# Kernel tuning notes

Hardware: AMD Instinct MI355X
Metric: run time of the kernel (lower is better)

The kernel has to match this reference:

```python
import jax, jax.numpy as jnp
import numpy as np

N = 50000        # total nodes (2 node types x 25000)
NPER = 25000     # nodes per type
E = 600000       # edges
R = 8            # num relations
NB = 4           # num bases
IND = 256        # raw input dim per node type
HID = 128        # hidden_dim
OUT = 64         # out_dim


def setup_inputs() -> dict:
    key = jax.random.key(0)
    ks = jax.random.split(key, 24)
    s_in = 1.0 / np.sqrt(IND)
    s_h = 1.0 / np.sqrt(HID)
    d = {
        "x_paper": jax.random.normal(ks[0], (NPER, IND), jnp.float32),
        "x_author": jax.random.normal(ks[1], (NPER, IND), jnp.float32),
        "W_paper": jax.random.normal(ks[2], (IND, HID), jnp.float32) * s_in,
        "b_paper": jnp.zeros((HID,), jnp.float32),
        "W_author": jax.random.normal(ks[3], (IND, HID), jnp.float32) * s_in,
        "b_author": jnp.zeros((HID,), jnp.float32),
        "bases0": jax.random.normal(ks[4], (NB, HID, HID), jnp.float32) * s_h,
        "comp0": jax.random.normal(ks[5], (R, NB), jnp.float32) * (1.0 / np.sqrt(NB)),
        "root0": jax.random.normal(ks[6], (HID, HID), jnp.float32) * s_h,
        "bias0": jnp.zeros((HID,), jnp.float32),
        "bases1": jax.random.normal(ks[7], (NB, HID, HID), jnp.float32) * s_h,
        "comp1": jax.random.normal(ks[8], (R, NB), jnp.float32) * (1.0 / np.sqrt(NB)),
        "root1": jax.random.normal(ks[9], (HID, HID), jnp.float32) * s_h,
        "bias1": jnp.zeros((HID,), jnp.float32),
        "bases2": jax.random.normal(ks[10], (NB, HID, OUT), jnp.float32) * s_h,
        "comp2": jax.random.normal(ks[11], (R, NB), jnp.float32) * (1.0 / np.sqrt(NB)),
        "root2": jax.random.normal(ks[12], (HID, OUT), jnp.float32) * s_h,
        "bias2": jnp.zeros((OUT,), jnp.float32),
        "edge_index": jax.random.randint(ks[13], (2, E), 0, N, dtype=jnp.int64),
        "edge_type": jax.random.randint(ks[14], (E,), 0, R, dtype=jnp.int64),
    }
    return d


def rgcn_conv(x, src, dst, etype, bases, comp, root, bias):
    # weight[r] = sum_b comp[r,b] * bases[b]  -> [R, in, out]
    W = jnp.einsum('rb,bio->rio', comp, bases)
    # per-(dst node, relation) mean aggregation (PyG RGCNConv default aggr='mean')
    seg = dst * R + etype                                   # [E]
    cnt = jax.ops.segment_sum(jnp.ones((E,), x.dtype), seg, num_segments=N * R)
    norm = 1.0 / jnp.maximum(cnt, 1.0)                      # [N*R]
    msg = x[src] * norm[seg][:, None]                       # [E, in]
    agg = jax.ops.segment_sum(msg, seg, num_segments=N * R) # [N*R, in]
    agg = agg.reshape(N, R, x.shape[1])                     # [N, R, in]
    return jnp.einsum('nri,rio->no', agg, W) + x @ root + bias


def reference(x_paper, x_author, W_paper, b_paper, W_author, b_author,
              bases0, comp0, root0, bias0,
              bases1, comp1, root1, bias1,
              bases2, comp2, root2, bias2,
              edge_index, edge_type):
    # Lazy linear projections + ReLU (dropout is identity in eval mode)
    hp = jax.nn.relu(x_paper @ W_paper + b_paper)
    ha = jax.nn.relu(x_author @ W_author + b_author)
    x = jnp.concatenate([hp, ha], axis=0)                   # [N, HID]

    src, dst = edge_index[0], edge_index[1]
    x_latents = [x]

    # conv 0 (i == 0: replace)
    h = jax.nn.relu(rgcn_conv(x, src, dst, edge_type, bases0, comp0, root0, bias0))
    x_latents.append(x)
    x = h

    # conv 1 (i > 0: residual add)
    h = jax.nn.relu(rgcn_conv(x, src, dst, edge_type, bases1, comp1, root1, bias1))
    x_latents.append(x)
    x = x + h

    # final conv
    out = rgcn_conv(x, src, dst, edge_type, bases2, comp2, root2, bias2)
    return (out, x_latents)
```

## Files before the change

kernel.cpp:

```cpp
#include <hip/hip_runtime.h>
#include <stdint.h>

#define NPER  25000
#define NNODE 50000
#define NEDGE 600000
#define NREL  8
#define NBASE 4
#define INDIM 256
#define HIDD  128
#define OUTD  64
#define NSEG  (NNODE * NREL)

typedef unsigned short u16;
typedef unsigned int   u32;
typedef __attribute__((ext_vector_type(8))) __bf16          bf16x8;
typedef __attribute__((ext_vector_type(8))) unsigned short  ushort8;
typedef __attribute__((ext_vector_type(4))) float           f32x4;

__device__ __forceinline__ u16 f2b(float f) {
    union { __bf16 h; u16 u; } v; v.h = (__bf16)f; return v.u;
}
__device__ __forceinline__ bf16x8 as_bf(ushort8 u) {
    union { ushort8 a; bf16x8 b; } v; v.a = u; return v.b;
}
__device__ __forceinline__ bf16x8 cvt8(const float* p) {
    f32x4 f0 = *(const f32x4*)p;
    f32x4 f1 = *(const f32x4*)(p + 4);
    ushort8 u;
#pragma unroll
    for (int i = 0; i < 4; i++) { u[i] = f2b(f0[i]); u[i + 4] = f2b(f1[i]); }
    return as_bf(u);
}
__device__ __forceinline__ float blo(u32 v) {
    union { u32 i; float f; } u; u.i = v << 16; return u.f;
}
__device__ __forceinline__ float bhi(u32 v) {
    union { u32 i; float f; } u; u.i = v & 0xffff0000u; return u.f;
}

__global__ void build_bsw_proj(const float* __restrict__ W, int K, u16* __restrict__ Bsw) {
    int idx = blockIdx.x * blockDim.x + threadIdx.x;
    if (idx >= K * 128) return;
    int j    = idx & 7;
    int lane = (idx >> 3) & 63;
    int rest = idx >> 9;
    int nt   = rest & 7;
    int ks   = rest >> 3;
    int col  = nt * 16 + (lane & 15);
    int k    = ks * 32 + ((lane >> 4) << 3) + j;
    Bsw[idx] = f2b(W[(size_t)k * 128 + col]);
}

__global__ void build_bsw_conv(const float* __restrict__ bases, const float* __restrict__ root,
                               int ncol, u16* __restrict__ Bsw) {
    int idx = blockIdx.x * blockDim.x + threadIdx.x;
    if (idx >= 640 * ncol) return;
    int nt_cnt = ncol >> 4;
    int j    = idx & 7;
    int lane = (idx >> 3) & 63;
    int rest = idx >> 9;
    int nt   = rest % nt_cnt;
    int ks   = rest / nt_cnt;
    int col  = nt * 16 + (lane & 15);
    int k    = ks * 32 + ((lane >> 4) << 3) + j;
    float v = (k < 512) ? bases[(size_t)k * ncol + col] : root[(size_t)(k - 512) * ncol + col];
    Bsw[idx] = f2b(v);
}

__global__ void hist_kernel(const int* __restrict__ ei, const int* __restrict__ et,
                            int* __restrict__ cnt) {
    int e = blockIdx.x * blockDim.x + threadIdx.x;
    if (e >= NEDGE) return;
    int dst = ei[NEDGE + e];
    int r   = et[e];
    atomicAdd(&cnt[dst * NREL + r], 1);
}

#define SCAN_CHUNK 1024
__global__ void scan1_kernel(int* __restrict__ data, int n, int* __restrict__ bsum) {
    __shared__ int sh[256];
    int t = threadIdx.x;
    int base = blockIdx.x * SCAN_CHUNK + t * 4;
    int v[4];
#pragma unroll
    for (int i = 0; i < 4; i++) v[i] = (base + i < n) ? data[base + i] : 0;
    int tot = v[0] + v[1] + v[2] + v[3];
    sh[t] = tot; __syncthreads();
    for (int off = 1; off < 256; off <<= 1) {
        int x = (t >= off) ? sh[t - off] : 0;
        __syncthreads();
        sh[t] += x;
        __syncthreads();
    }
    int excl = sh[t] - tot;
    if (t == 255) bsum[blockIdx.x] = sh[255];
    int run = excl;
#pragma unroll
    for (int i = 0; i < 4; i++) {
        if (base + i < n) data[base + i] = run;
        run += v[i];
    }
}

__global__ void scan2_kernel(int* __restrict__ bsum, int nb) {
    __shared__ int sh[512];
    int t = threadIdx.x;
    int v = (t < nb) ? bsum[t] : 0;
    sh[t] = v; __syncthreads();
    for (int off = 1; off < 512; off <<= 1) {
        int x = (t >= off) ? sh[t - off] : 0;
        __syncthreads();
        sh[t] += x;
        __syncthreads();
    }
    if (t < nb) bsum[t] = sh[t] - v;
}

__global__ void scan3_kernel(int* __restrict__ data, int n, const int* __restrict__ bsum) {
    int add = bsum[blockIdx.x];
    int base = blockIdx.x * SCAN_CHUNK + threadIdx.x * 4;
#pragma unroll
    for (int i = 0; i < 4; i++)
        if (base + i < n) data[base + i] += add;
}

__global__ void scatter_kernel(const int* __restrict__ ei, const int* __restrict__ et,
                               int* __restrict__ fill, int* __restrict__ epk) {
    int e = blockIdx.x * blockDim.x + threadIdx.x;
    if (e >= NEDGE) return;
    int src = ei[e];
    int dst = ei[NEDGE + e];
    int r   = et[e];
    int pos = atomicAdd(&fill[dst * NREL + r], 1);
    epk[pos] = src | (r << 16);
}

__global__ __launch_bounds__(256) void agg_kernel(
    const u16* __restrict__ xbf, const float* __restrict__ comp,
    const int* __restrict__ rowptr, const int* __restrict__ epk,
    u16* __restrict__ Abuf) {
    __shared__ float wtab[4][32];
    int tid  = threadIdx.x;
    int wv   = __builtin_amdgcn_readfirstlane(tid >> 6);
    int lane = tid & 63;
    int node = blockIdx.x * 4 + wv;
    int rbase = node * NREL;
    if (lane < 32) {
        int r  = lane >> 2;
        int c0 = rowptr[rbase + r], c1 = rowptr[rbase + r + 1];
        int cnt = c1 - c0;
        float nrm = (cnt > 0) ? 1.f / (float)cnt : 0.f;
        wtab[wv][lane] = comp[lane] * nrm;
    }
    __syncthreads();
    const float* wt = &wtab[wv][0];
    int p = rowptr[rbase];
    int e = rowptr[rbase + 8];
    int co = lane * 2;
    float a0[4] = {0.f, 0.f, 0.f, 0.f};
    float a1[4] = {0.f, 0.f, 0.f, 0.f};
    while (p + 4 <= e) {
        int k0 = epk[p], k1 = epk[p + 1], k2 = epk[p + 2], k3 = epk[p + 3];
        u32 v0 = *(const u32*)(xbf + ((size_t)(k0 & 0xffff) << 7) + co);
        u32 v1 = *(const u32*)(xbf + ((size_t)(k1 & 0xffff) << 7) + co);
        u32 v2 = *(const u32*)(xbf + ((size_t)(k2 & 0xffff) << 7) + co);
        u32 v3 = *(const u32*)(xbf + ((size_t)(k3 & 0xffff) << 7) + co);
        f32x4 w0 = *(const f32x4*)(wt + ((k0 >> 16) << 2));
        f32x4 w1 = *(const f32x4*)(wt + ((k1 >> 16) << 2));
        f32x4 w2 = *(const f32x4*)(wt + ((k2 >> 16) << 2));
        f32x4 w3 = *(const f32x4*)(wt + ((k3 >> 16) << 2));
        float x00 = blo(v0), x01 = bhi(v0);
        float x10 = blo(v1), x11 = bhi(v1);
        float x20 = blo(v2), x21 = bhi(v2);
        float x30 = blo(v3), x31 = bhi(v3);
#pragma unroll
        for (int b = 0; b < 4; b++) {
            a0[b] += w0[b] * x00; a1[b] += w0[b] * x01;
            a0[b] += w1[b] * x10; a1[b] += w1[b] * x11;
            a0[b] += w2[b] * x20; a1[b] += w2[b] * x21;
            a0[b] += w3[b] * x30; a1[b] += w3[b] * x31;
        }
        p += 4;
    }
    while (p < e) {
        int k0 = epk[p];
        u32 v0 = *(const u32*)(xbf + ((size_t)(k0 & 0xffff) << 7) + co);
        f32x4 w0 = *(const f32x4*)(wt + ((k0 >> 16) << 2));
        float x00 = blo(v0), x01 = bhi(v0);
#pragma unroll
        for (int b = 0; b < 4; b++) { a0[b] += w0[b] * x00; a1[b] += w0[b] * x01; }
        p++;
    }
    size_t ob = (size_t)node * 512 + co;
#pragma unroll
    for (int b = 0; b < 4; b++) {
        u32 pk = (u32)f2b(a0[b]) | ((u32)f2b(a1[b]) << 16);
        *(u32*)(Abuf + ob + b * 128) = pk;
    }
}

template<int KMAIN, bool HASX, int NT, bool RELU, bool RES, bool AF32>
__global__ __launch_bounds__(256) void gemm_kernel(
    const void* __restrict__ Av, const u16* __restrict__ xq,
    const u16* __restrict__ Bsw, const float* __restrict__ bias, int M,
    float* __restrict__ out1, float* __restrict__ out2, u16* __restrict__ outb,
    const float* __restrict__ resid, int ldo) {
    constexpr int KSM = KMAIN / 32;
    constexpr int KST = KSM + (HASX ? 4 : 0);
    int tid  = threadIdx.x;
    int wave = tid >> 6, lane = tid & 63;
    int l15  = lane & 15, quad = lane >> 4;
    int rowA = blockIdx.x * 64 + wave * 16 + l15;
    if (rowA > M - 1) rowA = M - 1;
    const u16* bp = Bsw + lane * 8;
    f32x4 acc[NT];
#pragma unroll
    for (int i = 0; i < NT; i++) acc[i] = (f32x4){0.f, 0.f, 0.f, 0.f};
#pragma unroll
    for (int ks = 0; ks < KST; ks++) {
        bf16x8 a;
        if (ks < KSM) {
            if (AF32) a = cvt8((const float*)Av + (size_t)rowA * KMAIN + ks * 32 + quad * 8);
            else      a = as_bf(*(const ushort8*)((const u16*)Av + (size_t)rowA * KMAIN + ks * 32 + quad * 8));
        } else {
            a = as_bf(*(const ushort8*)(xq + (size_t)rowA * 128 + (ks - KSM) * 32 + quad * 8));
        }
#pragma unroll
        for (int nt = 0; nt < NT; nt++) {
            bf16x8 b = as_bf(*(const ushort8*)(bp + ((size_t)(ks * NT + nt) << 9)));
            acc[nt] = __builtin_amdgcn_mfma_f32_16x16x32_bf16(a, b, acc[nt], 0, 0, 0);
        }
    }
    int orow0 = blockIdx.x * 64 + wave * 16 + quad * 4;
#pragma unroll
    for (int r = 0; r < 4; r++) {
        int orow = orow0 + r;
        if (orow < M) {
#pragma unroll
            for (int nt = 0; nt < NT; nt++) {
                int col = nt * 16 + l15;
                float v = acc[nt][r] + bias[col];
                if (RELU) v = v > 0.f ? v : 0.f;
                if (RES)  v += resid[(size_t)orow * ldo + col];
                size_t oi = (size_t)orow * ldo + col;
                if (out1) out1[oi] = v;
                if (out2) out2[oi] = v;
                if (outb) outb[oi] = f2b(v);
            }
        }
    }
}

extern "C" void kernel_launch(void* const* d_in, const int* in_sizes, int n_in,
                              void* d_out, int out_size, void* d_ws, size_t ws_size,
                              hipStream_t stream) {
    const float* x_paper  = (const float*)d_in[0];
    const float* x_author = (const float*)d_in[1];
    const float* W_paper  = (const float*)d_in[2];
    const float* b_paper  = (const float*)d_in[3];
    const float* W_author = (const float*)d_in[4];
    const float* b_author = (const float*)d_in[5];
    const float* bases0   = (const float*)d_in[6];
    const float* comp0    = (const float*)d_in[7];
    const float* root0    = (const float*)d_in[8];
    const float* bias0    = (const float*)d_in[9];
    const float* bases1   = (const float*)d_in[10];
    const float* comp1    = (const float*)d_in[11];
    const float* root1    = (const float*)d_in[12];
    const float* bias1    = (const float*)d_in[13];
    const float* bases2   = (const float*)d_in[14];
    const float* comp2    = (const float*)d_in[15];
    const float* root2    = (const float*)d_in[16];
    const float* bias2    = (const float*)d_in[17];
    const int* ei         = (const int*)d_in[18];
    const int* et         = (const int*)d_in[19];

    float* ob   = (float*)d_out;
    float* outF = ob;
    float* lat0 = ob + 3200000;
    float* lat1 = ob + 9600000;
    float* lat2 = ob + 16000000;

    char* w = (char*)d_ws;
    u16*   Abuf   = (u16*)(w + 0);
    u16*   xbf0   = (u16*)(w + 51200000);
    u16*   xbf1   = (u16*)(w + 64000000);
    u16*   Bswc   = (u16*)(w + 76800000);
    u16*   Bswp   = (u16*)(w + 76963840);
    u16*   Bswa   = (u16*)(w + 77029376);
    int*   rowptr = (int*)(w + 77094912);
    int*   fill   = (int*)(w + 78694976);
    int*   epk    = (int*)(w + 80294976);
    int*   bsum   = (int*)(w + 82694976);

    build_bsw_proj<<<(INDIM * HIDD + 255) / 256, 256, 0, stream>>>(W_paper, INDIM, Bswp);
    build_bsw_proj<<<(INDIM * HIDD + 255) / 256, 256, 0, stream>>>(W_author, INDIM, Bswa);
    gemm_kernel<256, false, 8, true, false, true><<<(NPER + 63) / 64, 256, 0, stream>>>(
        x_paper, nullptr, Bswp, b_paper, NPER, lat0, lat1, xbf0, nullptr, HIDD);
    gemm_kernel<256, false, 8, true, false, true><<<(NPER + 63) / 64, 256, 0, stream>>>(
        x_author, nullptr, Bswa, b_author, NPER,
        lat0 + (size_t)NPER * HIDD, lat1 + (size_t)NPER * HIDD,
        xbf0 + (size_t)NPER * HIDD, nullptr, HIDD);

    hipMemsetAsync(rowptr, 0, (NSEG + 1) * sizeof(int), stream);
    hist_kernel<<<(NEDGE + 255) / 256, 256, 0, stream>>>(ei, et, rowptr);
    int nchunk = (NSEG + 1 + SCAN_CHUNK - 1) / SCAN_CHUNK;
    scan1_kernel<<<nchunk, 256, 0, stream>>>(rowptr, NSEG + 1, bsum);
    scan2_kernel<<<1, 512, 0, stream>>>(bsum, nchunk);
    scan3_kernel<<<nchunk, 256, 0, stream>>>(rowptr, NSEG + 1, bsum);
    hipMemcpyAsync(fill, rowptr, NSEG * sizeof(int), hipMemcpyDeviceToDevice, stream);
    scatter_kernel<<<(NEDGE + 255) / 256, 256, 0, stream>>>(ei, et, fill, epk);

    build_bsw_conv<<<(640 * HIDD + 255) / 256, 256, 0, stream>>>(bases0, root0, HIDD, Bswc);
    agg_kernel<<<NNODE / 4, 256, 0, stream>>>(xbf0, comp0, rowptr, epk, Abuf);
    gemm_kernel<512, true, 8, true, false, false><<<(NNODE + 63) / 64, 256, 0, stream>>>(
        Abuf, xbf0, Bswc, bias0, NNODE, lat2, nullptr, xbf1, nullptr, HIDD);

    build_bsw_conv<<<(640 * HIDD + 255) / 256, 256, 0, stream>>>(bases1, root1, HIDD, Bswc);
    agg_kernel<<<NNODE / 4, 256, 0, stream>>>(xbf1, comp1, rowptr, epk, Abuf);
    gemm_kernel<512, true, 8, true, true, false><<<(NNODE + 63) / 64, 256, 0, stream>>>(
        Abuf, xbf1, Bswc, bias1, NNODE, nullptr, nullptr, xbf0, lat2, HIDD);

    build_bsw_conv<<<(640 * OUTD + 255) / 256, 256, 0, stream>>>(bases2, root2, OUTD, Bswc);
    agg_kernel<<<NNODE / 4, 256, 0, stream>>>(xbf0, comp2, rowptr, epk, Abuf);
    gemm_kernel<512, true, 4, false, false, false><<<(NNODE + 63) / 64, 256, 0, stream>>>(
        Abuf, xbf0, Bswc, bias2, NNODE, outF, nullptr, nullptr, nullptr, OUTD);
}
```

Baseline: 465.8 us.

## Merge weight prep and projections, pipeline aggregation loads, retile conv GEMMs

Puts all five weight-swizzle builds into one launch and both input projections into one 2D-grid launch. The rowptr-to-fill device copy is folded into the last scan pass. The aggregation loop is software-pipelined, prefetching the next four edges' indices and features while the current ones are accumulated, with padded invalid entries in place of a scalar tail loop. The conv GEMMs now run 2 waves per block with each wave computing two 16-row tiles, reusing each B fragment across both tiles at the cost of more registers per wave.

```diff
diff --git a/kernel.cpp b/kernel.cpp
--- a/kernel.cpp
+++ b/kernel.cpp
@@ -38,9 +38,7 @@
     union { u32 i; float f; } u; u.i = v & 0xffff0000u; return u.f;
 }
 
-__global__ void build_bsw_proj(const float* __restrict__ W, int K, u16* __restrict__ Bsw) {
-    int idx = blockIdx.x * blockDim.x + threadIdx.x;
-    if (idx >= K * 128) return;
+__device__ __forceinline__ void bsw_proj_elem(const float* __restrict__ W, u16* __restrict__ out, int idx) {
     int j    = idx & 7;
     int lane = (idx >> 3) & 63;
     int rest = idx >> 9;
@@ -48,13 +46,10 @@
     int ks   = rest >> 3;
     int col  = nt * 16 + (lane & 15);
     int k    = ks * 32 + ((lane >> 4) << 3) + j;
-    Bsw[idx] = f2b(W[(size_t)k * 128 + col]);
-}
-
-__global__ void build_bsw_conv(const float* __restrict__ bases, const float* __restrict__ root,
-                               int ncol, u16* __restrict__ Bsw) {
-    int idx = blockIdx.x * blockDim.x + threadIdx.x;
-    if (idx >= 640 * ncol) return;
+    out[idx] = f2b(W[(size_t)k * 128 + col]);
+}
+__device__ __forceinline__ void bsw_conv_elem(const float* __restrict__ bases, const float* __restrict__ root,
+                                              int ncol, u16* __restrict__ out, int idx) {
     int nt_cnt = ncol >> 4;
     int j    = idx & 7;
     int lane = (idx >> 3) & 63;
@@ -64,7 +59,20 @@
     int col  = nt * 16 + (lane & 15);
     int k    = ks * 32 + ((lane >> 4) << 3) + j;
     float v = (k < 512) ? bases[(size_t)k * ncol + col] : root[(size_t)(k - 512) * ncol + col];
-    Bsw[idx] = f2b(v);
+    out[idx] = f2b(v);
+}
+__global__ void build_bsw_all(const float* __restrict__ Wp, const float* __restrict__ Wa,
+                              const float* __restrict__ bases0, const float* __restrict__ root0,
+                              const float* __restrict__ bases1, const float* __restrict__ root1,
+                              const float* __restrict__ bases2, const float* __restrict__ root2,
+                              u16* __restrict__ Bswp, u16* __restrict__ Bswa,
+                              u16* __restrict__ Bswc0, u16* __restrict__ Bswc1, u16* __restrict__ Bswc2) {
+    int b = blockIdx.x, t = threadIdx.x;
+    if (b < 128)       bsw_proj_elem(Wp, Bswp, b * 256 + t);
+    else if (b < 256)  bsw_proj_elem(Wa, Bswa, (b - 128) * 256 + t);
+    else if (b < 576)  bsw_conv_elem(bases0, root0, HIDD, Bswc0, (b - 256) * 256 + t);
+    else if (b < 896)  bsw_conv_elem(bases1, root1, HIDD, Bswc1, (b - 576) * 256 + t);
+    else               bsw_conv_elem(bases2, root2, OUTD, Bswc2, (b - 896) * 256 + t);
 }
 
 __global__ void hist_kernel(const int* __restrict__ ei, const int* __restrict__ et,
@@ -116,12 +124,19 @@
     if (t < nb) bsum[t] = sh[t] - v;
 }
 
-__global__ void scan3_kernel(int* __restrict__ data, int n, const int* __restrict__ bsum) {
+__global__ void scan3_kernel(int* __restrict__ data, int n, const int* __restrict__ bsum,
+                             int* __restrict__ fill) {
     int add = bsum[blockIdx.x];
     int base = blockIdx.x * SCAN_CHUNK + threadIdx.x * 4;
 #pragma unroll
-    for (int i = 0; i < 4; i++)
-        if (base + i < n) data[base + i] += add;
+    for (int i = 0; i < 4; i++) {
+        int idx = base + i;
+        if (idx < n) {
+            int v = data[idx] + add;
+            data[idx] = v;
+            if (idx < NSEG) fill[idx] = v;
+        }
+    }
 }
 
 __global__ void scatter_kernel(const int* __restrict__ ei, const int* __restrict__ et,
@@ -139,57 +154,52 @@
     const u16* __restrict__ xbf, const float* __restrict__ comp,
     const int* __restrict__ rowptr, const int* __restrict__ epk,
     u16* __restrict__ Abuf) {
-    __shared__ float wtab[4][32];
+    __shared__ float wtab[4][40];
     int tid  = threadIdx.x;
     int wv   = __builtin_amdgcn_readfirstlane(tid >> 6);
     int lane = tid & 63;
     int node = blockIdx.x * 4 + wv;
     int rbase = node * NREL;
-    if (lane < 32) {
-        int r  = lane >> 2;
-        int c0 = rowptr[rbase + r], c1 = rowptr[rbase + r + 1];
-        int cnt = c1 - c0;
-        float nrm = (cnt > 0) ? 1.f / (float)cnt : 0.f;
-        wtab[wv][lane] = comp[lane] * nrm;
+    if (lane < 36) {
+        float wval = 0.f;
+        if (lane < 32) {
+            int r  = lane >> 2;
+            int c0 = rowptr[rbase + r], c1 = rowptr[rbase + r + 1];
+            int cnt = c1 - c0;
+            float nrm = (cnt > 0) ? 1.f / (float)cnt : 0.f;
+            wval = comp[lane] * nrm;
+        }
+        wtab[wv][lane] = wval;
     }
     __syncthreads();
     const float* wt = &wtab[wv][0];
-    int p = rowptr[rbase];
-    int e = rowptr[rbase + 8];
+    int p = __builtin_amdgcn_readfirstlane(rowptr[rbase]);
+    int e = __builtin_amdgcn_readfirstlane(rowptr[rbase + 8]);
     int co = lane * 2;
+    const int INV = 8 << 16;
     float a0[4] = {0.f, 0.f, 0.f, 0.f};
     float a1[4] = {0.f, 0.f, 0.f, 0.f};
-    while (p + 4 <= e) {
-        int k0 = epk[p], k1 = epk[p + 1], k2 = epk[p + 2], k3 = epk[p + 3];
-        u32 v0 = *(const u32*)(xbf + ((size_t)(k0 & 0xffff) << 7) + co);
-        u32 v1 = *(const u32*)(xbf + ((size_t)(k1 & 0xffff) << 7) + co);
-        u32 v2 = *(const u32*)(xbf + ((size_t)(k2 & 0xffff) << 7) + co);
-        u32 v3 = *(const u32*)(xbf + ((size_t)(k3 & 0xffff) << 7) + co);
-        f32x4 w0 = *(const f32x4*)(wt + ((k0 >> 16) << 2));
-        f32x4 w1 = *(const f32x4*)(wt + ((k1 >> 16) << 2));
-        f32x4 w2 = *(const f32x4*)(wt + ((k2 >> 16) << 2));
-        f32x4 w3 = *(const f32x4*)(wt + ((k3 >> 16) << 2));
-        float x00 = blo(v0), x01 = bhi(v0);
-        float x10 = blo(v1), x11 = bhi(v1);
-        float x20 = blo(v2), x21 = bhi(v2);
-        float x30 = blo(v3), x31 = bhi(v3);
-#pragma unroll
-        for (int b = 0; b < 4; b++) {
-            a0[b] += w0[b] * x00; a1[b] += w0[b] * x01;
-            a0[b] += w1[b] * x10; a1[b] += w1[b] * x11;
-            a0[b] += w2[b] * x20; a1[b] += w2[b] * x21;
-            a0[b] += w3[b] * x30; a1[b] += w3[b] * x31;
-        }
-        p += 4;
-    }
-    while (p < e) {
-        int k0 = epk[p];
-        u32 v0 = *(const u32*)(xbf + ((size_t)(k0 & 0xffff) << 7) + co);
-        f32x4 w0 = *(const f32x4*)(wt + ((k0 >> 16) << 2));
-        float x00 = blo(v0), x01 = bhi(v0);
-#pragma unroll
-        for (int b = 0; b < 4; b++) { a0[b] += w0[b] * x00; a1[b] += w0[b] * x01; }
-        p++;
+    int k0[4]; u32 v0[4];
+#pragma unroll
+    for (int i = 0; i < 4; i++) k0[i] = (p + i < e) ? epk[p + i] : INV;
+#pragma unroll
+    for (int i = 0; i < 4; i++) v0[i] = *(const u32*)(xbf + ((size_t)(k0[i] & 0xffff) << 7) + co);
+    for (int pc = p; pc < e; pc += 4) {
+        int pn = pc + 4;
+        int k1[4]; u32 v1[4];
+#pragma unroll
+        for (int i = 0; i < 4; i++) k1[i] = (pn + i < e) ? epk[pn + i] : INV;
+#pragma unroll
+        for (int i = 0; i < 4; i++) v1[i] = *(const u32*)(xbf + ((size_t)(k1[i] & 0xffff) << 7) + co);
+#pragma unroll
+        for (int i = 0; i < 4; i++) {
+            f32x4 w = *(const f32x4*)(wt + ((k0[i] >> 16) << 2));
+            float xl = blo(v0[i]), xh = bhi(v0[i]);
+#pragma unroll
+            for (int b = 0; b < 4; b++) { a0[b] += w[b] * xl; a1[b] += w[b] * xh; }
+        }
+#pragma unroll
+        for (int i = 0; i < 4; i++) { k0[i] = k1[i]; v0[i] = v1[i]; }
     }
     size_t ob = (size_t)node * 512 + co;
 #pragma unroll
@@ -199,9 +209,9 @@
     }
 }
 
-template<int KMAIN, bool HASX, int NT, bool RELU, bool RES, bool AF32>
-__global__ __launch_bounds__(256) void gemm_kernel(
-    const void* __restrict__ Av, const u16* __restrict__ xq,
+template<int KMAIN, bool HASX, int NW, int MW, int NT, bool RELU, bool RES, bool AF32>
+__device__ __forceinline__ void gemm_core(
+    int blk, const void* __restrict__ Av, const u16* __restrict__ xq,
     const u16* __restrict__ Bsw, const float* __restrict__ bias, int M,
     float* __restrict__ out1, float* __restrict__ out2, u16* __restrict__ outb,
     const float* __restrict__ resid, int ldo) {
@@ -210,45 +220,84 @@
     int tid  = threadIdx.x;
     int wave = tid >> 6, lane = tid & 63;
     int l15  = lane & 15, quad = lane >> 4;
-    int rowA = blockIdx.x * 64 + wave * 16 + l15;
-    if (rowA > M - 1) rowA = M - 1;
+    int rowbase = blk * (NW * MW * 16) + wave * (MW * 16);
+    int rA[MW];
+#pragma unroll
+    for (int m = 0; m < MW; m++) {
+        rA[m] = rowbase + m * 16 + l15;
+        if (rA[m] > M - 1) rA[m] = M - 1;
+    }
     const u16* bp = Bsw + lane * 8;
-    f32x4 acc[NT];
-#pragma unroll
-    for (int i = 0; i < NT; i++) acc[i] = (f32x4){0.f, 0.f, 0.f, 0.f};
+    f32x4 acc[MW][NT];
+#pragma unroll
+    for (int m = 0; m < MW; m++)
+#pragma unroll
+        for (int i = 0; i < NT; i++) acc[m][i] = (f32x4){0.f, 0.f, 0.f, 0.f};
 #pragma unroll
     for (int ks = 0; ks < KST; ks++) {
-        bf16x8 a;
-        if (ks < KSM) {
-            if (AF32) a = cvt8((const float*)Av + (size_t)rowA * KMAIN + ks * 32 + quad * 8);
-            else      a = as_bf(*(const ushort8*)((const u16*)Av + (size_t)rowA * KMAIN + ks * 32 + quad * 8));
-        } else {
-            a = as_bf(*(const ushort8*)(xq + (size_t)rowA * 128 + (ks - KSM) * 32 + quad * 8));
+        bf16x8 a[MW];
+#pragma unroll
+        for (int m = 0; m < MW; m++) {
+            if (ks < KSM) {
+                if (AF32) a[m] = cvt8((const float*)Av + (size_t)rA[m] * KMAIN + ks * 32 + quad * 8);
+                else      a[m] = as_bf(*(const ushort8*)((const u16*)Av + (size_t)rA[m] * KMAIN + ks * 32 + quad * 8));
+            } else {
+                a[m] = as_bf(*(const ushort8*)(xq + (size_t)rA[m] * 128 + (ks - KSM) * 32 + quad * 8));
+            }
         }
 #pragma unroll
         for (int nt = 0; nt < NT; nt++) {
             bf16x8 b = as_bf(*(const ushort8*)(bp + ((size_t)(ks * NT + nt) << 9)));
-            acc[nt] = __builtin_amdgcn_mfma_f32_16x16x32_bf16(a, b, acc[nt], 0, 0, 0);
-        }
-    }
-    int orow0 = blockIdx.x * 64 + wave * 16 + quad * 4;
-#pragma unroll
-    for (int r = 0; r < 4; r++) {
-        int orow = orow0 + r;
-        if (orow < M) {
-#pragma unroll
-            for (int nt = 0; nt < NT; nt++) {
-                int col = nt * 16 + l15;
-                float v = acc[nt][r] + bias[col];
-                if (RELU) v = v > 0.f ? v : 0.f;
-                if (RES)  v += resid[(size_t)orow * ldo + col];
-                size_t oi = (size_t)orow * ldo + col;
-                if (out1) out1[oi] = v;
-                if (out2) out2[oi] = v;
-                if (outb) outb[oi] = f2b(v);
+#pragma unroll
+            for (int m = 0; m < MW; m++)
+                acc[m][nt] = __builtin_amdgcn_mfma_f32_16x16x32_bf16(a[m], b, acc[m][nt], 0, 0, 0);
+        }
+    }
+#pragma unroll
+    for (int m = 0; m < MW; m++) {
+        int orow0 = rowbase + m * 16 + quad * 4;
+#pragma unroll
+        for (int r = 0; r < 4; r++) {
+            int orow = orow0 + r;
+            if (orow < M) {
+#pragma unroll
+                for (int nt = 0; nt < NT; nt++) {
+                    int col = nt * 16 + l15;
+                    float v = acc[m][nt][r] + bias[col];
+                    if (RELU) v = v > 0.f ? v : 0.f;
+                    if (RES)  v += resid[(size_t)orow * ldo + col];
+                    size_t oi = (size_t)orow * ldo + col;
+                    if (out1) out1[oi] = v;
+                    if (out2) out2[oi] = v;
+                    if (outb) outb[oi] = f2b(v);
+                }
             }
         }
     }
+}
+
+template<int KMAIN, bool HASX, int NW, int MW, int NT, bool RELU, bool RES, bool AF32>
+__global__ __launch_bounds__(NW * 64, 2) void gemm_kernel(
+    const void* __restrict__ Av, const u16* __restrict__ xq,
+    const u16* __restrict__ Bsw, const float* __restrict__ bias, int M,
+    float* __restrict__ out1, float* __restrict__ out2, u16* __restrict__ outb,
+    const float* __restrict__ resid, int ldo) {
+    gemm_core<KMAIN, HASX, NW, MW, NT, RELU, RES, AF32>(
+        blockIdx.x, Av, xq, Bsw, bias, M, out1, out2, outb, resid, ldo);
+}
+
+__global__ __launch_bounds__(256, 2) void proj2_kernel(
+    const float* __restrict__ xp, const float* __restrict__ xa,
+    const u16* __restrict__ Bswp, const u16* __restrict__ Bswa,
+    const float* __restrict__ bp, const float* __restrict__ ba,
+    float* __restrict__ lat0, float* __restrict__ lat1, u16* __restrict__ xbf0) {
+    int y = blockIdx.y;
+    const float* A    = y ? xa : xp;
+    const u16*   B    = y ? Bswa : Bswp;
+    const float* bias = y ? ba : bp;
+    size_t off = (size_t)y * NPER * HIDD;
+    gemm_core<256, false, 4, 1, 8, true, false, true>(
+        blockIdx.x, A, nullptr, B, bias, NPER, lat0 + off, lat1 + off, xbf0 + off, nullptr, HIDD);
 }
 
 extern "C" void kernel_launch(void* const* d_in, const int* in_sizes, int n_in,
@@ -285,44 +334,40 @@
     u16*   Abuf   = (u16*)(w + 0);
     u16*   xbf0   = (u16*)(w + 51200000);
     u16*   xbf1   = (u16*)(w + 64000000);
-    u16*   Bswc   = (u16*)(w + 76800000);
-    u16*   Bswp   = (u16*)(w + 76963840);
-    u16*   Bswa   = (u16*)(w + 77029376);
-    int*   rowptr = (int*)(w + 77094912);
-    int*   fill   = (int*)(w + 78694976);
-    int*   epk    = (int*)(w + 80294976);
-    int*   bsum   = (int*)(w + 82694976);
-
-    build_bsw_proj<<<(INDIM * HIDD + 255) / 256, 256, 0, stream>>>(W_paper, INDIM, Bswp);
-    build_bsw_proj<<<(INDIM * HIDD + 255) / 256, 256, 0, stream>>>(W_author, INDIM, Bswa);
-    gemm_kernel<256, false, 8, true, false, true><<<(NPER + 63) / 64, 256, 0, stream>>>(
-        x_paper, nullptr, Bswp, b_paper, NPER, lat0, lat1, xbf0, nullptr, HIDD);
-    gemm_kernel<256, false, 8, true, false, true><<<(NPER + 63) / 64, 256, 0, stream>>>(
-        x_author, nullptr, Bswa, b_author, NPER,
-        lat0 + (size_t)NPER * HIDD, lat1 + (size_t)NPER * HIDD,
-        xbf0 + (size_t)NPER * HIDD, nullptr, HIDD);
+    u16*   Bswc0  = (u16*)(w + 76800000);
+    u16*   Bswc1  = (u16*)(w + 76963840);
+    u16*   Bswc2  = (u16*)(w + 77127680);
+    u16*   Bswp   = (u16*)(w + 77209600);
+    u16*   Bswa   = (u16*)(w + 77275136);
+    int*   rowptr = (int*)(w + 77340672);
+    int*   fill   = (int*)(w + 78940736);
+    int*   epk    = (int*)(w + 80540736);
+    int*   bsum   = (int*)(w + 82940736);
+
+    build_bsw_all<<<1056, 256, 0, stream>>>(W_paper, W_author, bases0, root0,
+                                            bases1, root1, bases2, root2,
+                                            Bswp, Bswa, Bswc0, Bswc1, Bswc2);
+
+    proj2_kernel<<<dim3((NPER + 63) / 64, 2), 256, 0, stream>>>(
+        x_paper, x_author, Bswp, Bswa, b_paper, b_author, lat0, lat1, xbf0);
 
     hipMemsetAsync(rowptr, 0, (NSEG + 1) * sizeof(int), stream);
     hist_kernel<<<(NEDGE + 255) / 256, 256, 0, stream>>>(ei, et, rowptr);
     int nchunk = (NSEG + 1 + SCAN_CHUNK - 1) / SCAN_CHUNK;
     scan1_kernel<<<nchunk, 256, 0, stream>>>(rowptr, NSEG + 1, bsum);
     scan2_kernel<<<1, 512, 0, stream>>>(bsum, nchunk);
-    scan3_kernel<<<nchunk, 256, 0, stream>>>(rowptr, NSEG + 1, bsum);
-    hipMemcpyAsync(fill, rowptr, NSEG * sizeof(int), hipMemcpyDeviceToDevice, stream);
+    scan3_kernel<<<nchunk, 256, 0, stream>>>(rowptr, NSEG + 1, bsum, fill);
     scatter_kernel<<<(NEDGE + 255) / 256, 256, 0, stream>>>(ei, et, fill, epk);
 
-    build_bsw_conv<<<(640 * HIDD + 255) / 256, 256, 0, stream>>>(bases0, root0, HIDD, Bswc);
     agg_kernel<<<NNODE / 4, 256, 0, stream>>>(xbf0, comp0, rowptr, epk, Abuf);
-    gemm_kernel<512, true, 8, true, false, false><<<(NNODE + 63) / 64, 256, 0, stream>>>(
-        Abuf, xbf0, Bswc, bias0, NNODE, lat2, nullptr, xbf1, nullptr, HIDD);
-
-    build_bsw_conv<<<(640 * HIDD + 255) / 256, 256, 0, stream>>>(bases1, root1, HIDD, Bswc);
+    gemm_kernel<512, true, 2, 2, 8, true, false, false><<<(NNODE + 63) / 64, 128, 0, stream>>>(
+        Abuf, xbf0, Bswc0, bias0, NNODE, lat2, nullptr, xbf1, nullptr, HIDD);
+
     agg_kernel<<<NNODE / 4, 256, 0, stream>>>(xbf1, comp1, rowptr, epk, Abuf);
-    gemm_kernel<512, true, 8, true, true, false><<<(NNODE + 63) / 64, 256, 0, stream>>>(
-        Abuf, xbf1, Bswc, bias1, NNODE, nullptr, nullptr, xbf0, lat2, HIDD);
-
-    build_bsw_conv<<<(640 * OUTD + 255) / 256, 256, 0, stream>>>(bases2, root2, OUTD, Bswc);
+    gemm_kernel<512, true, 2, 2, 8, true, true, false><<<(NNODE + 63) / 64, 128, 0, stream>>>(
+        Abuf, xbf1, Bswc1, bias1, NNODE, nullptr, nullptr, xbf0, lat2, HIDD);
+
     agg_kernel<<<NNODE / 4, 256, 0, stream>>>(xbf0, comp2, rowptr, epk, Abuf);
-    gemm_kernel<512, true, 4, false, false, false><<<(NNODE + 63) / 64, 256, 0, stream>>>(
-        Abuf, xbf0, Bswc, bias2, NNODE, outF, nullptr, nullptr, nullptr, OUTD);
-}
+    gemm_kernel<512, true, 2, 2, 4, false, false, false><<<(NNODE + 63) / 64, 128, 0, stream>>>(
+        Abuf, xbf0, Bswc2, bias2, NNODE, outF, nullptr, nullptr, nullptr, OUTD);
+}
```

New measurement: 455.0 us. 2.3% less time.
